# Kernel tuning notes

Measured on AMD Instinct MI355X. Metric: run time of the kernel, lower is better.

## Reference

```python
import jax, jax.numpy as jnp
import numpy as np

N = 131072      # total nodes in batch
D = 128         # input_dim
K_EXP = 1024    # input_dim * num_conv_kernels
H = 512         # cluster_model_hidden_dim
NG = 4          # number of groups (sub-models)
F_SEG = 8192    # fine clusters (global_max_pool segments)
G_SEG = 32      # coarse graphs (InstanceNorm segments)
C = 16          # node_num_classes
EPS = 1e-5      # InstanceNorm eps


def setup_inputs() -> dict:
    key = jax.random.key(0)
    ks = jax.random.split(key, 8)
    x = jax.random.normal(ks[0], (N, D), jnp.float32)
    # disjoint partition of node indices into NG groups (gather/scatter dispatch)
    group_indices = jax.random.permutation(ks[1], N).reshape(NG, N // NG)
    # sorted segment ids, every segment non-empty
    pool_cluster_fine = (jnp.arange(N) // (N // F_SEG)).astype(jnp.int32)
    batch_cluster_coarse = (jnp.arange(F_SEG) // (F_SEG // G_SEG)).astype(jnp.int32)
    # per-group NodeModel params: expand D -> K_EXP, relu, project -> H
    W1 = jax.random.normal(ks[2], (NG, D, K_EXP), jnp.float32) * (1.0 / np.sqrt(D))
    b1 = jnp.zeros((NG, K_EXP), jnp.float32)
    W2 = jax.random.normal(ks[3], (NG, K_EXP, H), jnp.float32) * (1.0 / np.sqrt(K_EXP))
    b2 = jnp.zeros((NG, H), jnp.float32)
    # classifier (glorot weight, zero bias)
    w_out = jax.random.normal(ks[4], (H, C), jnp.float32) * np.sqrt(2.0 / (H + C))
    b_out = jnp.zeros((C,), jnp.float32)
    return {"x": x, "group_indices": group_indices,
            "pool_cluster_fine": pool_cluster_fine,
            "batch_cluster_coarse": batch_cluster_coarse,
            "W1": W1, "b1": b1, "W2": W2, "b2": b2,
            "w_out": w_out, "b_out": b_out}


def reference(x, group_indices, pool_cluster_fine, batch_cluster_coarse,
              W1, b1, W2, b2, w_out, b_out):
    # per-group gather -> sub-model -> scatter (vectorized over groups)
    xg = x[group_indices]                                   # [NG, N/NG, D]
    h = jax.nn.relu(jnp.einsum('gnd,gdk->gnk', xg, W1) + b1[:, None, :])
    og = jnp.einsum('gnk,gkh->gnh', h, W2) + b2[:, None, :]  # [NG, N/NG, H]
    new_feat = jnp.zeros((x.shape[0], H), x.dtype).at[group_indices.reshape(-1)].set(
        og.reshape(-1, H))                                   # [N, H]
    # global_max_pool over fine clusters
    emb = jax.ops.segment_max(new_feat, pool_cluster_fine,
                              num_segments=F_SEG, indices_are_sorted=True)  # [F, H]
    # PyG InstanceNorm(affine=False): per coarse-graph, per-channel standardization
    ones = jnp.ones((F_SEG, 1), emb.dtype)
    cnt = jax.ops.segment_sum(ones, batch_cluster_coarse,
                              num_segments=G_SEG, indices_are_sorted=True)  # [G,1]
    mean = jax.ops.segment_sum(emb, batch_cluster_coarse,
                               num_segments=G_SEG, indices_are_sorted=True) / cnt
    var = jax.ops.segment_sum(emb * emb, batch_cluster_coarse,
                              num_segments=G_SEG, indices_are_sorted=True) / cnt - mean ** 2
    normed = (emb - mean[batch_cluster_coarse]) * jax.lax.rsqrt(var[batch_cluster_coarse] + EPS)
    # dropout is identity in eval mode; classifier
    logits = normed @ w_out + b_out                          # [F, C]
    return logits
```

## Files before the change

kernel.cpp:

```cpp
#include <hip/hip_runtime.h>
#include <stdint.h>

typedef __bf16 bf16;
typedef bf16 bf16x4 __attribute__((ext_vector_type(4)));
typedef bf16 bf16x8 __attribute__((ext_vector_type(8)));
typedef float f32x4 __attribute__((ext_vector_type(4)));

#define N_NODES 131072
#define D_IN    128
#define KEXP    1024
#define H_DIM   512
#define NGRP    4
#define NPG     32768
#define F_SEG   8192
#define G_SEG   32
#define C_OUT   16

typedef const __attribute__((address_space(1))) void* gas_t;
typedef __attribute__((address_space(3))) void* las_t;
__device__ __forceinline__ void cp16_async(const bf16* g, bf16* l) {
    __builtin_amdgcn_global_load_lds((gas_t)g, (las_t)l, 16, 0, 0);
}

__global__ void convert_weights(const float* __restrict__ W1,
                                const float* __restrict__ W2,
                                bf16* __restrict__ W1F,
                                bf16* __restrict__ W2F)
{
    int t = blockIdx.x * 256 + threadIdx.x;
    if (t < 65536) {
        int slot = t & 63, f = (t >> 6) & 7, kc = (t >> 9) & 31, g = t >> 14;
        int ks = f >> 1, kt = f & 1, quad = slot >> 4, ln = slot & 15;
        int k = kc * 32 + kt * 16 + ln;
        const float* src = W1 + ((size_t)(g * 128 + ks * 32 + quad * 8)) * 1024 + k;
        bf16x8 v;
        #pragma unroll
        for (int j = 0; j < 8; ++j) v[j] = (bf16)src[(size_t)j * 1024];
        *(bf16x8*)(W1F + (size_t)t * 8) = v;
    } else {
        int u = t - 65536;
        if (u < 262144) {
            int slot = u & 63, f = (u >> 6) & 15, kc = (u >> 10) & 31;
            int n0t2 = (u >> 15) & 1, g = u >> 16;
            int quad = slot >> 4, ln = slot & 15;
            int k = kc * 32 + quad * 8;
            int n = n0t2 * 256 + f * 16 + ln;
            const float* src = W2 + ((size_t)(g * 1024 + k)) * 512 + n;
            bf16x8 v;
            #pragma unroll
            for (int j = 0; j < 8; ++j) v[j] = (bf16)src[(size_t)j * 512];
            *(bf16x8*)(W2F + (size_t)u * 8) = v;
        }
    }
}

__global__ __launch_bounds__(256, 2)
void mlp_kernel(const float* __restrict__ x,
                const int*   __restrict__ gidx,
                const bf16*  __restrict__ W1F,
                const float* __restrict__ b1,
                const bf16*  __restrict__ W2F,
                const float* __restrict__ b2,
                bf16*        __restrict__ NF)
{
    __shared__ __align__(16) bf16 sW1[2][4096];
    __shared__ __align__(16) bf16 sW2[2][8192];
    __shared__ __align__(16) bf16 sH[4096];

    const int tid  = threadIdx.x;
    const int bid  = blockIdx.x;
    const int g    = bid >> 9;
    const int rem  = bid & 511;
    const int m0   = (rem >> 1) * 128;
    const int n0t2 = rem & 1;

    const int wave = tid >> 6;
    const int lane = tid & 63;
    const int quad = lane >> 4;
    const int ln   = lane & 15;
    const int mg   = wave >> 1;
    const int ng   = wave & 1;

    const int*  gI  = gidx + g * NPG + m0;
    const bf16* W1g = W1F + (size_t)g * 131072;
    const bf16* W2g = W2F + (size_t)(g * 2 + n0t2) * 262144;
    const float* b1g = b1 + g * KEXP;

    bf16x8 xf[8];
    #pragma unroll
    for (int i = 0; i < 8; ++i) {
        int row  = wave * 32 + (i >> 2) * 16 + ln;
        int node = gI[row];
        const float* src = x + (size_t)node * D_IN + (i & 3) * 32 + quad * 8;
        float4 a = *(const float4*)src;
        float4 b = *(const float4*)(src + 4);
        bf16x8 v;
        v[0] = (bf16)a.x; v[1] = (bf16)a.y; v[2] = (bf16)a.z; v[3] = (bf16)a.w;
        v[4] = (bf16)b.x; v[5] = (bf16)b.y; v[6] = (bf16)b.z; v[7] = (bf16)b.w;
        xf[i] = v;
    }

    f32x4 acc2[4][8];
    #pragma unroll
    for (int a = 0; a < 4; ++a)
        #pragma unroll
        for (int b = 0; b < 8; ++b)
            acc2[a][b] = (f32x4){0.f, 0.f, 0.f, 0.f};

    #pragma unroll
    for (int r = 0; r < 2; ++r) {
        int c = r * 4 + wave;
        cp16_async(W1g + c * 512 + lane * 8, sW1[0] + c * 512);
    }
    #pragma unroll
    for (int r = 0; r < 4; ++r) {
        int c = r * 4 + wave;
        cp16_async(W2g + c * 512 + lane * 8, sW2[0] + c * 512);
    }

    #pragma unroll 1
    for (int kc = 0; kc < 32; ++kc) {
        __syncthreads();

        {
            int nkc = (kc + 1) & 31;
            const bf16* w2src = W2g + (size_t)nkc * 8192;
            bf16* d2 = sW2[(kc + 1) & 1];
            #pragma unroll
            for (int r = 0; r < 4; ++r) {
                int c = r * 4 + wave;
                cp16_async(w2src + c * 512 + lane * 8, d2 + c * 512);
            }
        }

        const bf16* w1buf = sW1[kc & 1];
        f32x4 acc1[2][2];
        #pragma unroll
        for (int a = 0; a < 2; ++a)
            #pragma unroll
            for (int b = 0; b < 2; ++b)
                acc1[a][b] = (f32x4){0.f, 0.f, 0.f, 0.f};

        #pragma unroll
        for (int ks = 0; ks < 4; ++ks) {
            #pragma unroll
            for (int kt = 0; kt < 2; ++kt) {
                bf16x8 w1f = *(const bf16x8*)(w1buf + ((ks * 2 + kt) * 64 + lane) * 8);
                #pragma unroll
                for (int mt = 0; mt < 2; ++mt)
                    acc1[kt][mt] = __builtin_amdgcn_mfma_f32_16x16x32_bf16(
                        w1f, xf[mt * 4 + ks], acc1[kt][mt], 0, 0, 0);
            }
        }

        #pragma unroll
        for (int kt = 0; kt < 2; ++kt) {
            float4 bv = *(const float4*)(b1g + kc * 32 + kt * 16 + quad * 4);
            float bvr[4] = {bv.x, bv.y, bv.z, bv.w};
            int qa = kt * 2 + (quad >> 1);
            int j0 = (quad & 1) * 4;
            #pragma unroll
            for (int mt = 0; mt < 2; ++mt) {
                int fm = wave * 2 + mt;
                bf16x4 pk;
                #pragma unroll
                for (int reg = 0; reg < 4; ++reg)
                    pk[reg] = (bf16)fmaxf(acc1[kt][mt][reg] + bvr[reg], 0.f);
                *(bf16x4*)(sH + (fm * 64 + qa * 16 + ln) * 8 + j0) = pk;
            }
        }

        __syncthreads();

        {
            int nkc = (kc + 1) & 31;
            const bf16* w1src = W1g + (size_t)nkc * 4096;
            bf16* d1 = sW1[(kc + 1) & 1];
            #pragma unroll
            for (int r = 0; r < 2; ++r) {
                int c = r * 4 + wave;
                cp16_async(w1src + c * 512 + lane * 8, d1 + c * 512);
            }
        }

        const bf16* w2buf = sW2[kc & 1];
        bf16x8 bb[8];
        #pragma unroll
        for (int nt = 0; nt < 8; ++nt)
            bb[nt] = *(const bf16x8*)(w2buf + ((ng * 8 + nt) * 64 + lane) * 8);
        #pragma unroll
        for (int mt = 0; mt < 4; ++mt) {
            bf16x8 a2 = *(const bf16x8*)(sH + ((mg * 4 + mt) * 64 + lane) * 8);
            #pragma unroll
            for (int nt = 0; nt < 8; ++nt)
                acc2[mt][nt] = __builtin_amdgcn_mfma_f32_16x16x32_bf16(
                    a2, bb[nt], acc2[mt][nt], 0, 0, 0);
        }
    }

    const float* b2g = b2 + g * H_DIM + n0t2 * 256 + ng * 128;
    float b2v[8];
    #pragma unroll
    for (int nt = 0; nt < 8; ++nt) b2v[nt] = b2g[nt * 16 + ln];

    #pragma unroll
    for (int mt = 0; mt < 4; ++mt)
        #pragma unroll
        for (int reg = 0; reg < 4; ++reg) {
            int row  = mg * 64 + mt * 16 + quad * 4 + reg;
            int node = gI[row];
            bf16* dst = NF + (size_t)node * H_DIM + n0t2 * 256 + ng * 128;
            #pragma unroll
            for (int nt = 0; nt < 8; ++nt)
                dst[nt * 16 + ln] = (bf16)(acc2[mt][nt][reg] + b2v[nt]);
        }
}

__global__ void pool_kernel(const bf16* __restrict__ NF, float* __restrict__ EMB)
{
    int t  = blockIdx.x * 256 + threadIdx.x;
    int f  = t >> 6;
    int c8 = (t & 63) * 8;
    const uint4* src = (const uint4*)(NF + (size_t)f * 16 * 512 + c8);
    float m[8];
    #pragma unroll
    for (int i = 0; i < 8; ++i) m[i] = -INFINITY;
    #pragma unroll
    for (int r = 0; r < 16; ++r) {
        uint4 v = src[(size_t)r * 64];
        uint32_t w[4] = {v.x, v.y, v.z, v.w};
        #pragma unroll
        for (int i = 0; i < 4; ++i) {
            m[2*i]   = fmaxf(m[2*i],   __uint_as_float(w[i] << 16));
            m[2*i+1] = fmaxf(m[2*i+1], __uint_as_float(w[i] & 0xffff0000u));
        }
    }
    float* dst = EMB + (size_t)f * 512 + c8;
    *(float4*)dst       = make_float4(m[0], m[1], m[2], m[3]);
    *(float4*)(dst + 4) = make_float4(m[4], m[5], m[6], m[7]);
}

__global__ void stats_kernel(const float* __restrict__ EMB,
                             float* __restrict__ MEAN,
                             float* __restrict__ RSIG)
{
    int gc = blockIdx.x;
    int ch = blockIdx.y * 128 + threadIdx.x;
    const float* p = EMB + (size_t)gc * 256 * 512 + ch;
    float s = 0.f, ss = 0.f;
    #pragma unroll 4
    for (int r = 0; r < 256; ++r) {
        float v = p[(size_t)r * 512];
        s += v; ss += v * v;
    }
    float mean = s * (1.f / 256.f);
    float var  = ss * (1.f / 256.f) - mean * mean;
    MEAN[gc * 512 + ch] = mean;
    RSIG[gc * 512 + ch] = rsqrtf(var + 1e-5f);
}

__global__ __launch_bounds__(256)
void classifier_kernel(const float* __restrict__ EMB,
                       const float* __restrict__ MEAN,
                       const float* __restrict__ RSIG,
                       const float* __restrict__ w_out,
                       const float* __restrict__ b_out,
                       float* __restrict__ out)
{
    __shared__ float sW[512 * 16];
    __shared__ float sE[16 * 513];
    int t  = threadIdx.x;
    int f0 = blockIdx.x * 16;
    int gc = f0 >> 8;

    #pragma unroll
    for (int it = 0; it < 8; ++it) {
        int i = (it * 256 + t) * 4;
        *(float4*)(sW + i) = *(const float4*)(w_out + i);
    }
    #pragma unroll
    for (int it = 0; it < 32; ++it) {
        int i  = it * 256 + t;
        int fr = i >> 9;
        int h  = i & 511;
        float v = EMB[(size_t)(f0 + fr) * 512 + h];
        sE[fr * 513 + h] = (v - MEAN[gc * 512 + h]) * RSIG[gc * 512 + h];
    }
    __syncthreads();

    int fr = t >> 4;
    int c  = t & 15;
    float acc = b_out[c];
    #pragma unroll 8
    for (int h = 0; h < 512; ++h)
        acc += sE[fr * 513 + h] * sW[h * 16 + c];
    out[(size_t)(f0 + fr) * 16 + c] = acc;
}

extern "C" void kernel_launch(void* const* d_in, const int* in_sizes, int n_in,
                              void* d_out, int out_size, void* d_ws, size_t ws_size,
                              hipStream_t stream)
{
    const float* x     = (const float*)d_in[0];
    const int*   gidx  = (const int*)d_in[1];
    const float* W1    = (const float*)d_in[4];
    const float* b1    = (const float*)d_in[5];
    const float* W2    = (const float*)d_in[6];
    const float* b2    = (const float*)d_in[7];
    const float* w_out = (const float*)d_in[8];
    const float* b_out = (const float*)d_in[9];
    float* out = (float*)d_out;

    char* w = (char*)d_ws;
    bf16* W1F = (bf16*)w;  w += (size_t)NGRP * KEXP * D_IN * 2;
    bf16* W2F = (bf16*)w;  w += (size_t)NGRP * H_DIM * KEXP * 2;
    bf16* NF  = (bf16*)w;  w += (size_t)N_NODES * H_DIM * 2;
    float* EMB  = (float*)w; w += (size_t)F_SEG * H_DIM * 4;
    float* MEAN = (float*)w; w += (size_t)G_SEG * H_DIM * 4;
    float* RSIG = (float*)w; w += (size_t)G_SEG * H_DIM * 4;

    convert_weights<<<1280, 256, 0, stream>>>(W1, W2, W1F, W2F);
    mlp_kernel<<<2048, 256, 0, stream>>>(x, gidx, W1F, b1, W2F, b2, NF);
    pool_kernel<<<2048, 256, 0, stream>>>(NF, EMB);
    stats_kernel<<<dim3(32, 4), 128, 0, stream>>>(EMB, MEAN, RSIG);
    classifier_kernel<<<512, 256, 0, stream>>>(EMB, MEAN, RSIG, w_out, b_out, out);
}
```

Before: 367.4 us.

## Software-pipeline stage1/stage2 with double-buffered hidden tile and direct W2 loads

```diff
diff --git a/kernel.cpp b/kernel.cpp
--- a/kernel.cpp
+++ b/kernel.cpp
@@ -64,8 +64,8 @@
                 bf16*        __restrict__ NF)
 {
     __shared__ __align__(16) bf16 sW1[2][4096];
-    __shared__ __align__(16) bf16 sW2[2][8192];
-    __shared__ __align__(16) bf16 sH[4096];
+    __shared__ __align__(16) bf16 sH[2][4096];
+    __shared__ __align__(16) float sB1[1024];
 
     const int tid  = threadIdx.x;
     const int bid  = blockIdx.x;
@@ -84,7 +84,6 @@
     const int*  gI  = gidx + g * NPG + m0;
     const bf16* W1g = W1F + (size_t)g * 131072;
     const bf16* W2g = W2F + (size_t)(g * 2 + n0t2) * 262144;
-    const float* b1g = b1 + g * KEXP;
 
     bf16x8 xf[8];
     #pragma unroll
@@ -100,6 +99,8 @@
         xf[i] = v;
     }
 
+    *(float4*)(sB1 + tid * 4) = *(const float4*)(b1 + g * KEXP + tid * 4);
+
     f32x4 acc2[4][8];
     #pragma unroll
     for (int a = 0; a < 4; ++a)
@@ -107,40 +108,15 @@
         for (int b = 0; b < 8; ++b)
             acc2[a][b] = (f32x4){0.f, 0.f, 0.f, 0.f};
 
-    #pragma unroll
-    for (int r = 0; r < 2; ++r) {
-        int c = r * 4 + wave;
-        cp16_async(W1g + c * 512 + lane * 8, sW1[0] + c * 512);
-    }
-    #pragma unroll
-    for (int r = 0; r < 4; ++r) {
-        int c = r * 4 + wave;
-        cp16_async(W2g + c * 512 + lane * 8, sW2[0] + c * 512);
-    }
-
-    #pragma unroll 1
-    for (int kc = 0; kc < 32; ++kc) {
-        __syncthreads();
-
-        {
-            int nkc = (kc + 1) & 31;
-            const bf16* w2src = W2g + (size_t)nkc * 8192;
-            bf16* d2 = sW2[(kc + 1) & 1];
-            #pragma unroll
-            for (int r = 0; r < 4; ++r) {
-                int c = r * 4 + wave;
-                cp16_async(w2src + c * 512 + lane * 8, d2 + c * 512);
-            }
-        }
-
-        const bf16* w1buf = sW1[kc & 1];
+    auto do_stage1 = [&](int j) {
+        const bf16* w1buf = sW1[j & 1];
+        bf16*       hdst  = sH[j & 1];
         f32x4 acc1[2][2];
         #pragma unroll
         for (int a = 0; a < 2; ++a)
             #pragma unroll
             for (int b = 0; b < 2; ++b)
                 acc1[a][b] = (f32x4){0.f, 0.f, 0.f, 0.f};
-
         #pragma unroll
         for (int ks = 0; ks < 4; ++ks) {
             #pragma unroll
@@ -152,10 +128,9 @@
                         w1f, xf[mt * 4 + ks], acc1[kt][mt], 0, 0, 0);
             }
         }
-
         #pragma unroll
         for (int kt = 0; kt < 2; ++kt) {
-            float4 bv = *(const float4*)(b1g + kc * 32 + kt * 16 + quad * 4);
+            float4 bv = *(const float4*)(sB1 + j * 32 + kt * 16 + quad * 4);
             float bvr[4] = {bv.x, bv.y, bv.z, bv.w};
             int qa = kt * 2 + (quad >> 1);
             int j0 = (quad & 1) * 4;
@@ -166,16 +141,44 @@
                 #pragma unroll
                 for (int reg = 0; reg < 4; ++reg)
                     pk[reg] = (bf16)fmaxf(acc1[kt][mt][reg] + bvr[reg], 0.f);
-                *(bf16x4*)(sH + (fm * 64 + qa * 16 + ln) * 8 + j0) = pk;
+                *(bf16x4*)(hdst + (fm * 64 + qa * 16 + ln) * 8 + j0) = pk;
             }
         }
-
+    };
+
+    __syncthreads();
+
+    #pragma unroll
+    for (int r = 0; r < 2; ++r) {
+        int c = r * 4 + wave;
+        cp16_async(W1g + c * 512 + lane * 8, sW1[0] + c * 512);
+    }
+    #pragma unroll
+    for (int r = 0; r < 2; ++r) {
+        int c = r * 4 + wave;
+        cp16_async(W1g + 4096 + c * 512 + lane * 8, sW1[1] + c * 512);
+    }
+    asm volatile("s_waitcnt vmcnt(2)" ::: "memory");
+    __builtin_amdgcn_s_barrier();
+
+    do_stage1(0);
+
+    #pragma unroll 1
+    for (int j = 1; j < 32; ++j) {
         __syncthreads();
 
+        bf16x8 bb[8];
         {
-            int nkc = (kc + 1) & 31;
+            const bf16* w2src = W2g + (size_t)(j - 1) * 8192 + ng * 4096;
+            #pragma unroll
+            for (int nt = 0; nt < 8; ++nt)
+                bb[nt] = *(const bf16x8*)(w2src + nt * 512 + lane * 8);
+        }
+
+        {
+            int nkc = (j + 1) & 31;
             const bf16* w1src = W1g + (size_t)nkc * 4096;
-            bf16* d1 = sW1[(kc + 1) & 1];
+            bf16* d1 = sW1[(j + 1) & 1];
             #pragma unroll
             for (int r = 0; r < 2; ++r) {
                 int c = r * 4 + wave;
@@ -183,14 +186,34 @@
             }
         }
 
-        const bf16* w2buf = sW2[kc & 1];
+        __builtin_amdgcn_s_setprio(1);
+        do_stage1(j);
+
+        {
+            const bf16* hbuf = sH[(j - 1) & 1];
+            #pragma unroll
+            for (int mt = 0; mt < 4; ++mt) {
+                bf16x8 a2 = *(const bf16x8*)(hbuf + ((mg * 4 + mt) * 64 + lane) * 8);
+                #pragma unroll
+                for (int nt = 0; nt < 8; ++nt)
+                    acc2[mt][nt] = __builtin_amdgcn_mfma_f32_16x16x32_bf16(
+                        a2, bb[nt], acc2[mt][nt], 0, 0, 0);
+            }
+        }
+        __builtin_amdgcn_s_setprio(0);
+    }
+
+    __syncthreads();
+    {
         bf16x8 bb[8];
+        const bf16* w2src = W2g + (size_t)31 * 8192 + ng * 4096;
         #pragma unroll
         for (int nt = 0; nt < 8; ++nt)
-            bb[nt] = *(const bf16x8*)(w2buf + ((ng * 8 + nt) * 64 + lane) * 8);
+            bb[nt] = *(const bf16x8*)(w2src + nt * 512 + lane * 8);
+        const bf16* hbuf = sH[1];
         #pragma unroll
         for (int mt = 0; mt < 4; ++mt) {
-            bf16x8 a2 = *(const bf16x8*)(sH + ((mg * 4 + mt) * 64 + lane) * 8);
+            bf16x8 a2 = *(const bf16x8*)(hbuf + ((mg * 4 + mt) * 64 + lane) * 8);
             #pragma unroll
             for (int nt = 0; nt < 8; ++nt)
                 acc2[mt][nt] = __builtin_amdgcn_mfma_f32_16x16x32_bf16(
```

Measured after the change: 358.2 us. -2.5%, faster.
